# Kernel tuning notes

Measured on AMD Instinct MI355X. Metric: run time of the kernel, lower is better.

## Reference

```python
import jax, jax.numpy as jnp
import numpy as np

B, F, V, D = 4096, 8, 1000, 1024  # batch, n_fields, vocab per field, hidden_size
LN_EPS = 1e-5


def layer_norm(x, g, b, eps=LN_EPS):
    mu = x.mean(axis=-1, keepdims=True)
    var = ((x - mu) ** 2).mean(axis=-1, keepdims=True)
    return (x - mu) * jax.lax.rsqrt(var + eps) * g + b


def setup_inputs() -> dict:
    key = jax.random.key(0)
    k0, k1, k2, k3 = jax.random.split(key, 4)
    return {
        "input_embedding": jax.random.normal(k0, (B, D), jnp.float32),
        "features": jax.random.randint(k1, (B, F), 0, V),
        "embed_tables": jax.random.normal(k2, (F, V, D), jnp.float32) * 0.02,
        "ln_gamma": jnp.ones((D,), jnp.float32),
        "ln_beta": jnp.zeros((D,), jnp.float32),
        "pred_W": jax.random.normal(k3, (F, D, V), jnpp := jnp.float32) * 0.02,
        "pred_b": jnp.zeros((F, V), jnp.float32),
    }


def reference(input_embedding, features, embed_tables, ln_gamma, ln_beta, pred_W, pred_b):
    # Per-field embedding lookup: (B, F, D)
    feat_emb = embed_tables[jnp.arange(F)[None, :], features]
    # Stack input embedding first, as in torch.stack([input_embedding] + ...):
    embeddings = jnp.concatenate([input_embedding[:, None, :], feat_emb], axis=1)  # (B, F+1, D)
    # triu(diagonal=1) masked broadcast-sum then [:, 1:, :] == exclusive causal prefix sum:
    # masked_sums[:, j] = sum_{i < j+1} embeddings[:, i] for j = 0..F-1
    masked_sums = jnp.cumsum(embeddings, axis=1)[:, :F, :]  # (B, F, D)
    h = jax.nn.gelu(layer_norm(masked_sums, ln_gamma, ln_beta), approximate=False)
    # Per-field predictor heads (Linear(D, V)), batched over fields:
    logits = jnp.einsum("bfd,fdv->bfv", h, pred_W) + pred_b  # (B, F, V)
    return logits
```

## Files before the change

### kernel.cpp

```cpp
#include <hip/hip_runtime.h>
#include <hip/hip_bf16.h>

#define B_ 4096
#define F_ 8
#define V_ 1000
#define D_ 1024
#define VP 1024

typedef __bf16 bf16x8 __attribute__((ext_vector_type(8)));
typedef float f32x4 __attribute__((ext_vector_type(4)));

__device__ __forceinline__ void gload_lds16(const void* g, void* l) {
  __builtin_amdgcn_global_load_lds(
      (const __attribute__((address_space(1))) void*)g,
      (__attribute__((address_space(3))) void*)l, 16, 0, 0);
}

__device__ __forceinline__ float gelu_fast(float x) {
  float z = 0.7978845608028654f * (x + 0.044715f * x * x * x);
  z = fminf(fmaxf(z, -9.0f), 9.0f);
  float e = __expf(2.0f * z);
  float t = (e - 1.0f) / (e + 1.0f);
  return 0.5f * x * (1.0f + t);
}

__global__ __launch_bounds__(256) void transpose_w(
    const float* __restrict__ W, __hip_bfloat16* __restrict__ Wt) {
  __shared__ float tile[64][65];
  const int id = blockIdx.x;
  const int f = id >> 8;
  const int v0 = ((id >> 4) & 15) * 64;
  const int k0 = (id & 15) * 64;
  const int t = threadIdx.x;
  const int tx = t & 15;
  const int ty = t >> 4;
  const float* Wf = W + (size_t)f * D_ * V_;
#pragma unroll
  for (int p = 0; p < 4; ++p) {
    int k = k0 + ty + p * 16;
    int v = v0 + tx * 4;
    float4 val;
    if (v + 3 < V_) {
      val = *reinterpret_cast<const float4*>(&Wf[(size_t)k * V_ + v]);
    } else {
      val.x = (v + 0 < V_) ? Wf[(size_t)k * V_ + v + 0] : 0.0f;
      val.y = (v + 1 < V_) ? Wf[(size_t)k * V_ + v + 1] : 0.0f;
      val.z = (v + 2 < V_) ? Wf[(size_t)k * V_ + v + 2] : 0.0f;
      val.w = (v + 3 < V_) ? Wf[(size_t)k * V_ + v + 3] : 0.0f;
    }
    tile[ty + p * 16][tx * 4 + 0] = val.x;
    tile[ty + p * 16][tx * 4 + 1] = val.y;
    tile[ty + p * 16][tx * 4 + 2] = val.z;
    tile[ty + p * 16][tx * 4 + 3] = val.w;
  }
  __syncthreads();
  __hip_bfloat16* Wtf = Wt + (size_t)f * VP * D_;
#pragma unroll
  for (int p = 0; p < 4; ++p) {
    int vr = ty + p * 16;
    int kc = tx * 4;
    __hip_bfloat16 hb[4];
#pragma unroll
    for (int j = 0; j < 4; ++j)
      hb[j] = __float2bfloat16(tile[kc + j][vr]);
    *reinterpret_cast<uint2*>(&Wtf[(size_t)(v0 + vr) * D_ + k0 + kc]) =
        *reinterpret_cast<const uint2*>(hb);
  }
}

__global__ __launch_bounds__(256) void fuse_h(
    const float* __restrict__ emb, const int* __restrict__ feats,
    const float* __restrict__ tables, const float* __restrict__ gamma,
    const float* __restrict__ beta, __hip_bfloat16* __restrict__ H) {
  const int t = threadIdx.x;
  const int wave = t >> 6, lane = t & 63;
  const int b = blockIdx.x * 4 + wave;

  float s[16];
#pragma unroll
  for (int j = 0; j < 4; ++j) {
    float4 v = *reinterpret_cast<const float4*>(
        &emb[(size_t)b * D_ + lane * 4 + j * 256]);
    s[j * 4 + 0] = v.x; s[j * 4 + 1] = v.y;
    s[j * 4 + 2] = v.z; s[j * 4 + 3] = v.w;
  }
  float gm[16], bt[16];
#pragma unroll
  for (int j = 0; j < 4; ++j) {
    float4 g = *reinterpret_cast<const float4*>(&gamma[lane * 4 + j * 256]);
    float4 bb = *reinterpret_cast<const float4*>(&beta[lane * 4 + j * 256]);
    gm[j * 4 + 0] = g.x; gm[j * 4 + 1] = g.y;
    gm[j * 4 + 2] = g.z; gm[j * 4 + 3] = g.w;
    bt[j * 4 + 0] = bb.x; bt[j * 4 + 1] = bb.y;
    bt[j * 4 + 2] = bb.z; bt[j * 4 + 3] = bb.w;
  }

  float4 nxt[4];
  {
    int feat = feats[b * F_ + 0];
    const float* row = tables + ((size_t)0 * V_ + feat) * D_;
#pragma unroll
    for (int j = 0; j < 4; ++j)
      nxt[j] = *reinterpret_cast<const float4*>(&row[lane * 4 + j * 256]);
  }

  for (int f = 0; f < F_; ++f) {
    float sum = 0.0f, ssq = 0.0f;
#pragma unroll
    for (int j = 0; j < 16; ++j) {
      sum += s[j];
      ssq += s[j] * s[j];
    }
#pragma unroll
    for (int off = 32; off > 0; off >>= 1) {
      sum += __shfl_xor(sum, off, 64);
      ssq += __shfl_xor(ssq, off, 64);
    }
    const float mu = sum * (1.0f / D_);
    const float var = ssq * (1.0f / D_) - mu * mu;
    const float rstd = rsqrtf(var + 1e-5f);

    __hip_bfloat16* Hrow = H + (size_t)f * (B_ * D_) + (size_t)b * D_;
#pragma unroll
    for (int j = 0; j < 4; ++j) {
      __hip_bfloat16 hb[4];
#pragma unroll
      for (int q = 0; q < 4; ++q) {
        float x = (s[j * 4 + q] - mu) * rstd * gm[j * 4 + q] + bt[j * 4 + q];
        hb[q] = __float2bfloat16(gelu_fast(x));
      }
      *reinterpret_cast<uint2*>(&Hrow[lane * 4 + j * 256]) =
          *reinterpret_cast<const uint2*>(hb);
    }

    if (f < F_ - 1) {
      float4 cur[4];
#pragma unroll
      for (int j = 0; j < 4; ++j) cur[j] = nxt[j];
      if (f < F_ - 2) {
        int feat = feats[b * F_ + f + 1];
        const float* row = tables + ((size_t)(f + 1) * V_ + feat) * D_;
#pragma unroll
        for (int j = 0; j < 4; ++j)
          nxt[j] = *reinterpret_cast<const float4*>(&row[lane * 4 + j * 256]);
      }
#pragma unroll
      for (int j = 0; j < 4; ++j) {
        s[j * 4 + 0] += cur[j].x; s[j * 4 + 1] += cur[j].y;
        s[j * 4 + 2] += cur[j].z; s[j * 4 + 3] += cur[j].w;
      }
    }
  }
}

#define AOFF 0
#define BOFF 32768

#define STAGE(OPB, GB, DBUF, HALF, KT)                                        \
  do {                                                                        \
    const ushort* _g = (GB) + (size_t)(HALF) * (128 * D_) + (size_t)(KT) * 64;\
    ushort* _l = &lds[(OPB) + ((DBUF)*2 + (HALF)) * 8192 + w * 512];          \
    gload_lds16(_g, _l);                                                      \
    gload_lds16(_g + 64 * D_, _l + 4096);                                     \
  } while (0)

#define LD_A(DST, LBASE, FIOFF)                                               \
  _Pragma("unroll") for (int _fj = 0; _fj < 4; ++_fj)                         \
  _Pragma("unroll") for (int _ks = 0; _ks < 2; ++_ks)                         \
      DST[_fj][_ks] = *reinterpret_cast<const bf16x8*>(                       \
          (LBASE) + ((((FIOFF) + _fj) * 2 + _ks) * 512));

#define LD_B(DST, LBASE, NFOFF)                                               \
  _Pragma("unroll") for (int _fn = 0; _fn < 2; ++_fn)                         \
  _Pragma("unroll") for (int _ks = 0; _ks < 2; ++_ks)                         \
      DST[_fn][_ks] = *reinterpret_cast<const bf16x8*>(                       \
          (LBASE) + ((((NFOFF) + _fn) * 2 + _ks) * 512));

#define Q_MFMA(AF, BF, R0, C0)                                                \
  do {                                                                        \
    __builtin_amdgcn_s_setprio(1);                                            \
    _Pragma("unroll") for (int _fj = 0; _fj < 4; ++_fj)                       \
    _Pragma("unroll") for (int _fn = 0; _fn < 2; ++_fn)                       \
    _Pragma("unroll") for (int _ks = 0; _ks < 2; ++_ks)                       \
        acc[(R0) + _fj][(C0) + _fn] =                                         \
            __builtin_amdgcn_mfma_f32_16x16x32_bf16(                          \
                AF[_fj][_ks], BF[_fn][_ks], acc[(R0) + _fj][(C0) + _fn],      \
                0, 0, 0);                                                     \
    __builtin_amdgcn_s_setprio(0);                                            \
  } while (0)

#define PHB                                                                   \
  do {                                                                        \
    asm volatile("" ::: "memory");                                            \
    __builtin_amdgcn_s_barrier();                                             \
    asm volatile("" ::: "memory");                                            \
  } while (0)

#define WAITV6 asm volatile("s_waitcnt vmcnt(6)" ::: "memory")
#define WAITV0 asm volatile("s_waitcnt vmcnt(0)" ::: "memory")

__global__ __launch_bounds__(512, 2) void gemm_hw(
    const ushort* __restrict__ H,
    const ushort* __restrict__ Wt,
    const float* __restrict__ bias,
    float* __restrict__ out) {
  __shared__ ushort lds[65536];

  const int bid = blockIdx.x;
  const int swz = (bid & 7) * 64 + (bid >> 3);
  const int f = swz >> 6;
  const int r = swz & 63;
  const int mt = r >> 2, nt = r & 3;

  const int t = threadIdx.x;
  const int w = t >> 6, l = t & 63;
  const int wm = w >> 2;
  const int wn = w & 3;

  const ushort* Hf = H + (size_t)f * (B_ * D_);
  const ushort* Wf = Wt + (size_t)f * (VP * D_);

  const int srow = ((w >> 1) << 4) + (l >> 2);
  const int skx = ((w & 1) << 5) + ((((l & 3) << 3)) ^ (((l >> 5) & 1) << 4));
  const ushort* gA = Hf + (size_t)(mt * 256 + srow) * D_ + skx;
  const ushort* gB = Wf + (size_t)(nt * 256 + srow) * D_ + skx;

  const int laneu =
      ((l & 15) << 5) + (((((l >> 4) << 4)) ^ (((l >> 3) & 1) << 5)) >> 1);
  const ushort* lA[2] = {&lds[(0 * 2 + wm) * 8192 + laneu],
                         &lds[(1 * 2 + wm) * 8192 + laneu]};
  const ushort* lB[2] = {
      &lds[BOFF + (0 * 2 + (wn >> 1)) * 8192 + (wn & 1) * 4096 + laneu],
      &lds[BOFF + (1 * 2 + (wn >> 1)) * 8192 + (wn & 1) * 4096 + laneu]};

  bf16x8 a0[4][2], a1[4][2], b0[2][2], b1[2][2];
  f32x4 acc[8][4] = {};

  STAGE(AOFF, gA, 0, 0, 0);
  STAGE(AOFF, gA, 0, 1, 0);
  STAGE(BOFF, gB, 0, 0, 0);
  STAGE(BOFF, gB, 0, 1, 0);
  STAGE(AOFF, gA, 1, 0, 1);
  STAGE(AOFF, gA, 1, 1, 1);
  STAGE(BOFF, gB, 1, 0, 1);
  WAITV6;
  PHB;

#pragma unroll 1
  for (int i = 0; i < 8; ++i) {
    const int t1 = 2 * i + 1, t2 = 2 * i + 2, t3 = 2 * i + 3;
    const bool more = (i < 7);
    LD_A(a0, lA[0], 0);
    LD_B(b0, lB[0], 0);
    STAGE(BOFF, gB, 1, 1, t1);
    PHB;
    Q_MFMA(a0, b0, 0, 0);
    LD_A(a1, lA[0], 4);
    if (more) STAGE(AOFF, gA, 0, 0, t2);
    PHB;
    Q_MFMA(a1, b0, 4, 0);
    LD_B(b1, lB[0], 2);
    if (more) STAGE(AOFF, gA, 0, 1, t2);
    PHB;
    Q_MFMA(a0, b1, 0, 2);
    if (more) STAGE(BOFF, gB, 0, 0, t2);
    if (more) { WAITV6; } else { WAITV0; }
    PHB;
    Q_MFMA(a1, b1, 4, 2);
    LD_A(a0, lA[1], 0);
    LD_B(b0, lB[1], 0);
    if (more) STAGE(BOFF, gB, 0, 1, t2);
    PHB;
    Q_MFMA(a0, b0, 0, 0);
    LD_A(a1, lA[1], 4);
    if (more) STAGE(AOFF, gA, 1, 0, t3);
    PHB;
    Q_MFMA(a1, b0, 4, 0);
    LD_B(b1, lB[1], 2);
    if (more) STAGE(AOFF, gA, 1, 1, t3);
    PHB;
    Q_MFMA(a0, b1, 0, 2);
    if (more) {
      STAGE(BOFF, gB, 1, 0, t3);
      WAITV6;
    }
    PHB;
    Q_MFMA(a1, b1, 4, 2);
  }

  const float* bp = bias + f * V_;
  const int orow0 = mt * 256 + wm * 128 + ((l >> 4) << 2);
  const int ocol0 = nt * 256 + wn * 64 + (l & 15);
#pragma unroll
  for (int fi = 0; fi < 8; ++fi) {
#pragma unroll
    for (int fn = 0; fn < 4; ++fn) {
      int col = ocol0 + fn * 16;
      if (col < V_) {
        float bb = bp[col];
        int row = orow0 + fi * 16;
        float* op = out + (size_t)row * (F_ * V_) + (size_t)f * V_ + col;
#pragma unroll
        for (int q = 0; q < 4; ++q)
          op[(size_t)q * (F_ * V_)] = acc[fi][fn][q] + bb;
      }
    }
  }
}

extern "C" void kernel_launch(void* const* d_in, const int* in_sizes, int n_in,
                              void* d_out, int out_size, void* d_ws,
                              size_t ws_size, hipStream_t stream) {
  const float* emb = (const float*)d_in[0];
  const int* feats = (const int*)d_in[1];
  const float* tables = (const float*)d_in[2];
  const float* gamma = (const float*)d_in[3];
  const float* beta = (const float*)d_in[4];
  const float* W = (const float*)d_in[5];
  const float* bias = (const float*)d_in[6];
  float* out = (float*)d_out;

  char* ws = (char*)d_ws;
  __hip_bfloat16* Hbuf = (__hip_bfloat16*)ws;
  __hip_bfloat16* Wtbuf =
      (__hip_bfloat16*)(ws + (size_t)F_ * B_ * D_ * 2);

  transpose_w<<<dim3(2048), dim3(256), 0, stream>>>(W, Wtbuf);
  fuse_h<<<dim3(1024), dim3(256), 0, stream>>>(emb, feats, tables, gamma,
                                               beta, Hbuf);
  gemm_hw<<<dim3((B_ / 256) * (VP / 256) * F_), dim3(512), 0, stream>>>(
      (const ushort*)Hbuf, (const ushort*)Wtbuf, bias, out);
}
```

Measured before the change: 128.5 us.

## Replace double-buffered 8-phase GEMM pipeline with single-buffer load-all-then-compute loop

The GEMM main loop drops its LDS double buffering and the interleaved eight-phase schedule, which had a barrier between each MFMA quarter. Each iteration now loads all A/B fragments into registers, waits on LDS, issues the next tile's global-to-LDS copies, runs all MFMAs, then waits for the copies to finish. This halves LDS use to 64KB per block and removes most barriers, which may help occupancy and cut sync overhead. The cost is that global loads overlap only with one tile's MFMAs and every iteration ends in a full vmcnt(0) stall, and fragments held in registers raise register pressure.

After: 131.1 us. 2.1% more time.

```diff
diff --git a/kernel.cpp b/kernel.cpp
--- a/kernel.cpp
+++ b/kernel.cpp
@@ -153,13 +153,18 @@
   }
 }
 
-#define AOFF 0
-#define BOFF 32768
-
-#define STAGE(OPB, GB, DBUF, HALF, KT)                                        \
+#define STAGE_A(HALF, KT)                                                     \
   do {                                                                        \
-    const ushort* _g = (GB) + (size_t)(HALF) * (128 * D_) + (size_t)(KT) * 64;\
-    ushort* _l = &lds[(OPB) + ((DBUF)*2 + (HALF)) * 8192 + w * 512];          \
+    const ushort* _g = gA + (size_t)(HALF) * (128 * D_) + (size_t)(KT) * 64;  \
+    ushort* _l = &lds[(HALF)*8192 + w * 512];                                 \
+    gload_lds16(_g, _l);                                                      \
+    gload_lds16(_g + 64 * D_, _l + 4096);                                     \
+  } while (0)
+
+#define STAGE_B(HALF, KT)                                                     \
+  do {                                                                        \
+    const ushort* _g = gB + (size_t)(HALF) * (128 * D_) + (size_t)(KT) * 64;  \
+    ushort* _l = &lds[16384 + (HALF)*8192 + w * 512];                         \
     gload_lds16(_g, _l);                                                      \
     gload_lds16(_g + 64 * D_, _l + 4096);                                     \
   } while (0)
@@ -189,22 +194,23 @@
     __builtin_amdgcn_s_setprio(0);                                            \
   } while (0)
 
-#define PHB                                                                   \
+#define BARRIER                                                               \
   do {                                                                        \
     asm volatile("" ::: "memory");                                            \
     __builtin_amdgcn_s_barrier();                                             \
     asm volatile("" ::: "memory");                                            \
   } while (0)
 
-#define WAITV6 asm volatile("s_waitcnt vmcnt(6)" ::: "memory")
+#define SB0 __builtin_amdgcn_sched_barrier(0)
 #define WAITV0 asm volatile("s_waitcnt vmcnt(0)" ::: "memory")
+#define WAITLG0 asm volatile("s_waitcnt lgkmcnt(0)" ::: "memory")
 
 __global__ __launch_bounds__(512, 2) void gemm_hw(
     const ushort* __restrict__ H,
     const ushort* __restrict__ Wt,
     const float* __restrict__ bias,
     float* __restrict__ out) {
-  __shared__ ushort lds[65536];
+  __shared__ ushort lds[32768];
 
   const int bid = blockIdx.x;
   const int swz = (bid & 7) * 64 + (bid >> 3);
@@ -227,65 +233,44 @@
 
   const int laneu =
       ((l & 15) << 5) + (((((l >> 4) << 4)) ^ (((l >> 3) & 1) << 5)) >> 1);
-  const ushort* lA[2] = {&lds[(0 * 2 + wm) * 8192 + laneu],
-                         &lds[(1 * 2 + wm) * 8192 + laneu]};
-  const ushort* lB[2] = {
-      &lds[BOFF + (0 * 2 + (wn >> 1)) * 8192 + (wn & 1) * 4096 + laneu],
-      &lds[BOFF + (1 * 2 + (wn >> 1)) * 8192 + (wn & 1) * 4096 + laneu]};
+  const ushort* lA = &lds[wm * 8192 + laneu];
+  const ushort* lB = &lds[16384 + (wn >> 1) * 8192 + (wn & 1) * 4096 + laneu];
 
   bf16x8 a0[4][2], a1[4][2], b0[2][2], b1[2][2];
   f32x4 acc[8][4] = {};
 
-  STAGE(AOFF, gA, 0, 0, 0);
-  STAGE(AOFF, gA, 0, 1, 0);
-  STAGE(BOFF, gB, 0, 0, 0);
-  STAGE(BOFF, gB, 0, 1, 0);
-  STAGE(AOFF, gA, 1, 0, 1);
-  STAGE(AOFF, gA, 1, 1, 1);
-  STAGE(BOFF, gB, 1, 0, 1);
-  WAITV6;
-  PHB;
+  STAGE_A(0, 0);
+  STAGE_A(1, 0);
+  STAGE_B(0, 0);
+  STAGE_B(1, 0);
+  WAITV0;
+  BARRIER;
 
 #pragma unroll 1
-  for (int i = 0; i < 8; ++i) {
-    const int t1 = 2 * i + 1, t2 = 2 * i + 2, t3 = 2 * i + 3;
-    const bool more = (i < 7);
-    LD_A(a0, lA[0], 0);
-    LD_B(b0, lB[0], 0);
-    STAGE(BOFF, gB, 1, 1, t1);
-    PHB;
+  for (int T = 0; T < 16; ++T) {
+    const int tn = T + 1;
+    const bool more = (T < 15);
+    LD_A(a0, lA, 0);
+    LD_A(a1, lA, 4);
+    LD_B(b0, lB, 0);
+    LD_B(b1, lB, 2);
+    SB0;
+    WAITLG0;
+    BARRIER;
+    if (more) {
+      STAGE_A(0, tn);
+      STAGE_A(1, tn);
+      STAGE_B(0, tn);
+      STAGE_B(1, tn);
+    }
+    SB0;
     Q_MFMA(a0, b0, 0, 0);
-    LD_A(a1, lA[0], 4);
-    if (more) STAGE(AOFF, gA, 0, 0, t2);
-    PHB;
     Q_MFMA(a1, b0, 4, 0);
-    LD_B(b1, lB[0], 2);
-    if (more) STAGE(AOFF, gA, 0, 1, t2);
-    PHB;
     Q_MFMA(a0, b1, 0, 2);
-    if (more) STAGE(BOFF, gB, 0, 0, t2);
-    if (more) { WAITV6; } else { WAITV0; }
-    PHB;
     Q_MFMA(a1, b1, 4, 2);
-    LD_A(a0, lA[1], 0);
-    LD_B(b0, lB[1], 0);
-    if (more) STAGE(BOFF, gB, 0, 1, t2);
-    PHB;
-    Q_MFMA(a0, b0, 0, 0);
-    LD_A(a1, lA[1], 4);
-    if (more) STAGE(AOFF, gA, 1, 0, t3);
-    PHB;
-    Q_MFMA(a1, b0, 4, 0);
-    LD_B(b1, lB[1], 2);
-    if (more) STAGE(AOFF, gA, 1, 1, t3);
-    PHB;
-    Q_MFMA(a0, b1, 0, 2);
-    if (more) {
-      STAGE(BOFF, gB, 1, 0, t3);
-      WAITV6;
-    }
-    PHB;
-    Q_MFMA(a1, b1, 4, 2);
+    SB0;
+    WAITV0;
+    BARRIER;
   }
 
   const float* bp = bias + f * V_;
```
